# Kernel tuning notes

Measured on AMD Instinct MI355X. Metric: run time of the kernel, lower is better.

Reference implementation:

```python
import jax, jax.numpy as jnp
import numpy as np

N, E, D, R, L = 50000, 250000, 256, 8, 3


def setup_inputs() -> dict:
    key = jax.random.key(0)
    k = jax.random.split(key, 7)
    scale = 1.0 / np.sqrt(D)
    x = jax.random.normal(k[0], (N, D), dtype=jnp.float32)
    edge_index = jax.random.randint(k[1], (2, E), 0, N, dtype=jnp.int64)
    edge_type = jax.random.randint(k[2], (E,), 0, R, dtype=jnp.int64)
    W_rel = jax.random.normal(k[3], (L, R, D, D), dtype=jnp.float32) * scale
    W_root = jax.random.normal(k[4], (L, D, D), dtype=jnp.float32) * scale
    bias = jax.random.normal(k[5], (L, D), dtype=jnp.float32) * 0.02
    return {"x": x, "edge_index": edge_index, "edge_type": edge_type,
            "W_rel": W_rel, "W_root": W_root, "bias": bias}


def reference(x, edge_index, edge_type, W_rel, W_root, bias):
    # RGCNEncoder on the flattened (offset-concatenated) graph:
    # L layers of: h = relu( x @ W_root + b + scatter_add_dst( W_rel[rt] @ x[src] ) )
    src, dst = edge_index[0], edge_index[1]
    n_layers = W_rel.shape[0]
    for l in range(n_layers):  # small fixed layer loop
        # per-relation transform of ALL nodes, then gather per edge by (relation, src)
        xr = jnp.einsum('nd,rde->rne', x, W_rel[l])        # [R, N, D]
        msg = xr[edge_type, src]                           # [E, D] gather
        agg = jax.ops.segment_sum(msg, dst, num_segments=x.shape[0])  # scatter-add
        x = jax.nn.relu(agg + x @ W_root[l] + bias[l])
    return x
```

## Files before the change

kernel.cpp:

```cpp
#include <hip/hip_runtime.h>

#define NN 50000
#define NE 250000
#define DD 256
#define NREL 8
#define NL 3

#define NSRCB ((NN + 127) / 128)
#define NBKT (NREL * NSRCB)

typedef __attribute__((ext_vector_type(8))) short short8;
typedef __attribute__((ext_vector_type(4))) float floatx4;
typedef __attribute__((ext_vector_type(2))) unsigned int u32x2;

#if __has_builtin(__builtin_amdgcn_global_load_lds)
#define GLOAD16(g, l) __builtin_amdgcn_global_load_lds( \
    (__attribute__((address_space(1))) void*)(void*)(g), \
    (__attribute__((address_space(3))) void*)(void*)(l), 16, 0, 0)
#else
#define GLOAD16(g, l) do { *(uint4*)(l) = *(const uint4*)(g); } while (0)
#endif

__device__ inline unsigned short f2bf(float f) {
    unsigned int u = __builtin_bit_cast(unsigned int, f);
    u += 0x7FFFu + ((u >> 16) & 1u);
    return (unsigned short)(u >> 16);
}
__device__ inline float bf2f(unsigned short u) {
    unsigned int x = ((unsigned int)u) << 16;
    return __builtin_bit_cast(float, x);
}

__global__ void zero_ints(int* __restrict__ p, int n) {
    int i = blockIdx.x * blockDim.x + threadIdx.x;
    if (i < n) p[i] = 0;
}

__global__ void hist_bkt(const int* __restrict__ ei, const int* __restrict__ et,
                         int* __restrict__ bktCnt) {
    int e = blockIdx.x * blockDim.x + threadIdx.x;
    if (e < NE) atomicAdd(&bktCnt[et[e] * NSRCB + (ei[e] >> 7)], 1);
}

__global__ __launch_bounds__(256)
void scan_part(const int* __restrict__ cnt, int n, int* __restrict__ blockSums) {
    __shared__ int ps[256];
    const int b = blockIdx.x, t = threadIdx.x;
    const int base = b * 1024 + t * 4;
    int s = 0;
#pragma unroll
    for (int j = 0; j < 4; ++j) s += (base + j < n) ? cnt[base + j] : 0;
    ps[t] = s;
    __syncthreads();
    for (int o = 128; o > 0; o >>= 1) {
        if (t < o) ps[t] += ps[t + o];
        __syncthreads();
    }
    if (t == 0) blockSums[b] = ps[0];
}

__global__ __launch_bounds__(256)
void scan_tops(const int* __restrict__ blockSums, int nb, int* __restrict__ blockOffs) {
    __shared__ int ps[256];
    const int t = threadIdx.x;
    ps[t] = (t < nb) ? blockSums[t] : 0;
    __syncthreads();
    for (int o = 1; o < 256; o <<= 1) {
        int x = (t >= o) ? ps[t - o] : 0;
        __syncthreads();
        ps[t] += x;
        __syncthreads();
    }
    blockOffs[t] = (t == 0) ? 0 : ps[t - 1];
}

__global__ __launch_bounds__(256)
void scan_local(const int* __restrict__ cnt, int n, int total,
                const int* __restrict__ blockOffs,
                int* __restrict__ offs, int* __restrict__ cur) {
    __shared__ int ps[256];
    const int b = blockIdx.x, t = threadIdx.x;
    const int base = b * 1024 + t * 4;
    int v[4];
#pragma unroll
    for (int j = 0; j < 4; ++j) v[j] = (base + j < n) ? cnt[base + j] : 0;
    int s = v[0] + v[1] + v[2] + v[3];
    ps[t] = s;
    __syncthreads();
    for (int o = 1; o < 256; o <<= 1) {
        int x = (t >= o) ? ps[t - o] : 0;
        __syncthreads();
        ps[t] += x;
        __syncthreads();
    }
    int run = blockOffs[b] + ((t == 0) ? 0 : ps[t - 1]);
#pragma unroll
    for (int j = 0; j < 4; ++j) {
        if (base + j < n) { offs[base + j] = run; cur[base + j] = run; run += v[j]; }
    }
    if (b == 0 && t == 0) offs[n] = total;
}

__global__ void mk_reloffs(const int* __restrict__ bktOff, int* __restrict__ relOffs) {
    const int t = threadIdx.x;
    if (t < NREL) relOffs[t] = bktOff[t * NSRCB];
    if (t == 0) relOffs[NREL] = NE;
}

__global__ void scatter_bkt(const int* __restrict__ ei, const int* __restrict__ et,
                            int* __restrict__ bktCur, int* __restrict__ ssrc,
                            int* __restrict__ sdst) {
    int e = blockIdx.x * blockDim.x + threadIdx.x;
    if (e < NE) {
        int s = ei[e];
        int p = atomicAdd(&bktCur[et[e] * NSRCB + (s >> 7)], 1);
        ssrc[p] = s;
        sdst[p] = ei[NE + e];
    }
}

__global__ void hist_dst(const int* __restrict__ sdst, int* __restrict__ dstCnt) {
    int p = blockIdx.x * blockDim.x + threadIdx.x;
    if (p < NE) atomicAdd(&dstCnt[sdst[p]], 1);
}

__global__ void mk_mpos(const int* __restrict__ sdst, int* __restrict__ dstCur,
                        int* __restrict__ mpos) {
    int p = blockIdx.x * blockDim.x + threadIdx.x;
    if (p < NE) mpos[p] = atomicAdd(&dstCur[sdst[p]], 1);
}

__global__ void transpose_bf16(const float* __restrict__ src, unsigned short* __restrict__ dst) {
    __shared__ float t[32][33];
    const size_t mb = (size_t)blockIdx.x * DD * DD;
    const int d0 = blockIdx.y * 32, e0 = blockIdx.z * 32;
    const int tx = threadIdx.x, ty = threadIdx.y;
#pragma unroll
    for (int i = 0; i < 4; ++i)
        t[ty + 8 * i][tx] = src[mb + (size_t)(d0 + ty + 8 * i) * DD + e0 + tx];
    __syncthreads();
#pragma unroll
    for (int i = 0; i < 4; ++i)
        dst[mb + (size_t)(e0 + ty + 8 * i) * DD + d0 + tx] = f2bf(t[tx][ty + 8 * i]);
}

__global__ void conv_bf16(const float4* __restrict__ s, ushort4* __restrict__ d, int n4) {
    int i = blockIdx.x * blockDim.x + threadIdx.x;
    const int stride = gridDim.x * blockDim.x;
    for (; i < n4; i += stride) {
        float4 v = s[i];
        d[i] = make_ushort4(f2bf(v.x), f2bf(v.y), f2bf(v.z), f2bf(v.w));
    }
}

__global__ void relu_convert(float4* __restrict__ p, ushort4* __restrict__ xb, int n4) {
    int i = blockIdx.x * blockDim.x + threadIdx.x;
    const int stride = gridDim.x * blockDim.x;
    for (; i < n4; i += stride) {
        float4 v = p[i];
        v.x = v.x > 0.f ? v.x : 0.f;
        v.y = v.y > 0.f ? v.y : 0.f;
        v.z = v.z > 0.f ? v.z : 0.f;
        v.w = v.w > 0.f ? v.w : 0.f;
        p[i] = v;
        xb[i] = make_ushort4(f2bf(v.x), f2bf(v.y), f2bf(v.z), f2bf(v.w));
    }
}

__global__ __launch_bounds__(256)
void root_gemm_r(const unsigned short* __restrict__ Xb, const unsigned short* __restrict__ WT,
                 const float* __restrict__ bias, float* __restrict__ Cf,
                 unsigned short* __restrict__ Cb, int useB)
{
    __shared__ unsigned short As[128][32];
    __shared__ unsigned short Bs[128][32];
    const int tid = threadIdx.x;
    const int lane = tid & 63;
    const int w = tid >> 6;
    const int wr = w >> 1, wc = w & 1;
    const int m0 = blockIdx.x * 128;
    const int n0 = blockIdx.y * 128;
    const int srow = tid >> 2;
    const int sq = tid & 3;

    floatx4 acc[4][4] = {};

    for (int kt = 0; kt < DD / 32; ++kt) {
        const int k0 = kt * 32;
        int r0 = min(m0 + srow, NN - 1);
        int r1 = min(m0 + srow + 64, NN - 1);
        GLOAD16(&Xb[(size_t)r0 * DD + k0 + sq * 8], &As[srow][sq * 8]);
        GLOAD16(&Xb[(size_t)r1 * DD + k0 + sq * 8], &As[srow + 64][sq * 8]);
        GLOAD16(&WT[(size_t)(n0 + srow) * DD + k0 + sq * 8], &Bs[srow][sq * 8]);
        GLOAD16(&WT[(size_t)(n0 + srow + 64) * DD + k0 + sq * 8], &Bs[srow + 64][sq * 8]);
        __syncthreads();
        short8 a[4], b[4];
#pragma unroll
        for (int mi = 0; mi < 4; ++mi)
            a[mi] = *(const short8*)&As[wr * 64 + mi * 16 + (lane & 15)][(lane >> 4) * 8];
#pragma unroll
        for (int ni = 0; ni < 4; ++ni)
            b[ni] = *(const short8*)&Bs[wc * 64 + ni * 16 + (lane & 15)][(lane >> 4) * 8];
#pragma unroll
        for (int mi = 0; mi < 4; ++mi)
#pragma unroll
            for (int ni = 0; ni < 4; ++ni)
                acc[mi][ni] = __builtin_amdgcn_mfma_f32_16x16x32_bf16(a[mi], b[ni], acc[mi][ni], 0, 0, 0);
        __syncthreads();
    }

    const int cq = lane >> 4;
    const int cn = lane & 15;
#pragma unroll
    for (int mi = 0; mi < 4; ++mi) {
#pragma unroll
        for (int q = 0; q < 4; ++q) {
            int row = m0 + wr * 64 + mi * 16 + cq * 4 + q;
            if (row < NN) {
#pragma unroll
                for (int ni = 0; ni < 4; ++ni) {
                    int col = n0 + wc * 64 + ni * 16 + cn;
                    float val = acc[mi][ni][q] + bias[col];
                    if (useB) Cb[(size_t)row * DD + col] = f2bf(val);
                    else      Cf[(size_t)row * DD + col] = val;
                }
            }
        }
    }
}

__global__ __launch_bounds__(256)
void edge_msgs_m(const unsigned short* __restrict__ Xb, const unsigned short* __restrict__ WTl,
                 const int* __restrict__ ssrc, const int* __restrict__ mpos,
                 const int* __restrict__ relOffs, unsigned short* __restrict__ msgs)
{
    __shared__ unsigned short As[128][32];
    __shared__ unsigned short Bs[128][32];
    __shared__ int srcs[128];
    __shared__ int mposs[128];

    const int t = blockIdx.x;
    int rel = -1, base = 0, cnt = 0, accT = 0;
#pragma unroll
    for (int r = 0; r < NREL; ++r) {
        int s = relOffs[r], e = relOffs[r + 1];
        int nt = (e - s + 127) / 128;
        if (rel < 0 && t < accT + nt) {
            rel = r;
            base = s + (t - accT) * 128;
            cnt = min(128, e - base);
        }
        accT += nt;
    }
    if (rel < 0) return;

    const int tid = threadIdx.x;
    if (tid < 128) {
        int idx = base + tid;
        srcs[tid] = (tid < cnt) ? ssrc[idx] : 0;
        mposs[tid] = (tid < cnt) ? mpos[idx] : 0;
    }
    __syncthreads();

    const unsigned short* WT = WTl + (size_t)rel * DD * DD;

    const int lane = tid & 63;
    const int w = tid >> 6;
    const int wr = w >> 1, wc = w & 1;
    const int n0 = blockIdx.y * 128;
    const int srow = tid >> 2;
    const int sq = tid & 3;

    floatx4 acc[4][4] = {};

    for (int kt = 0; kt < DD / 32; ++kt) {
        const int k0 = kt * 32;
        int r0 = srcs[srow];
        int r1 = srcs[srow + 64];
        GLOAD16(&Xb[(size_t)r0 * DD + k0 + sq * 8], &As[srow][sq * 8]);
        GLOAD16(&Xb[(size_t)r1 * DD + k0 + sq * 8], &As[srow + 64][sq * 8]);
        GLOAD16(&WT[(size_t)(n0 + srow) * DD + k0 + sq * 8], &Bs[srow][sq * 8]);
        GLOAD16(&WT[(size_t)(n0 + srow + 64) * DD + k0 + sq * 8], &Bs[srow + 64][sq * 8]);
        __syncthreads();
        short8 a[4], b[4];
#pragma unroll
        for (int mi = 0; mi < 4; ++mi)
            a[mi] = *(const short8*)&As[wr * 64 + mi * 16 + (lane & 15)][(lane >> 4) * 8];
#pragma unroll
        for (int ni = 0; ni < 4; ++ni)
            b[ni] = *(const short8*)&Bs[wc * 64 + ni * 16 + (lane & 15)][(lane >> 4) * 8];
#pragma unroll
        for (int mi = 0; mi < 4; ++mi)
#pragma unroll
            for (int ni = 0; ni < 4; ++ni)
                acc[mi][ni] = __builtin_amdgcn_mfma_f32_16x16x32_bf16(a[mi], b[ni], acc[mi][ni], 0, 0, 0);
        __syncthreads();
    }

    const int cq = lane >> 4;
    const int cn = lane & 15;
#pragma unroll
    for (int mi = 0; mi < 4; ++mi) {
#pragma unroll
        for (int q = 0; q < 4; ++q) {
            int slot = wr * 64 + mi * 16 + cq * 4 + q;
            if (slot < cnt) {
                size_t mrow = (size_t)mposs[slot] * DD + n0 + wc * 64;
#pragma unroll
                for (int ni = 0; ni < 4; ++ni)
                    msgs[mrow + ni * 16 + cn] = f2bf(acc[mi][ni][q]);
            }
        }
    }
}

__global__ __launch_bounds__(256)
void combine4b(const unsigned short* __restrict__ msgs, const int* __restrict__ dstOffs,
               const unsigned short* __restrict__ rootb, const float* __restrict__ rootf,
               float* __restrict__ out, unsigned short* __restrict__ xb,
               int useRootB, int last)
{
    int v = blockIdx.x * 4 + (threadIdx.x >> 6);
    if (v >= NN) return;
    const int lane = threadIdx.x & 63;
    const size_t rb = (size_t)v * DD + lane * 4;
    float4 a;
    if (useRootB) {
        u32x2 r = *(const u32x2*)&rootb[rb];
        a.x = bf2f((unsigned short)(r.x & 0xffff));
        a.y = bf2f((unsigned short)(r.x >> 16));
        a.z = bf2f((unsigned short)(r.y & 0xffff));
        a.w = bf2f((unsigned short)(r.y >> 16));
    } else {
        a = *(const float4*)&rootf[rb];
    }
    const int b0 = dstOffs[v], b1 = dstOffs[v + 1];
    for (int k = b0; k < b1; ++k) {
        u32x2 m = *(const u32x2*)&msgs[(size_t)k * DD + lane * 4];
        a.x += bf2f((unsigned short)(m.x & 0xffff));
        a.y += bf2f((unsigned short)(m.x >> 16));
        a.z += bf2f((unsigned short)(m.y & 0xffff));
        a.w += bf2f((unsigned short)(m.y >> 16));
    }
    a.x = a.x > 0.f ? a.x : 0.f;
    a.y = a.y > 0.f ? a.y : 0.f;
    a.z = a.z > 0.f ? a.z : 0.f;
    a.w = a.w > 0.f ? a.w : 0.f;
    if (last) {
        *(float4*)&out[rb] = a;
    } else {
        *(ushort4*)&xb[rb] = make_ushort4(f2bf(a.x), f2bf(a.y), f2bf(a.z), f2bf(a.w));
    }
}

__global__ __launch_bounds__(256)
void edge_gemm_mfma(const unsigned short* __restrict__ Xb, const unsigned short* __restrict__ WTl,
                    const int* __restrict__ ssrc, const int* __restrict__ sdst,
                    const int* __restrict__ offsets, float* __restrict__ out)
{
    __shared__ unsigned short As[128][32];
    __shared__ unsigned short Bs[128][32];
    __shared__ int srcs[128];
    __shared__ int dsts[128];

    const int t = blockIdx.x;
    int rel = -1, base = 0, cnt = 0, accT = 0;
#pragma unroll
    for (int r = 0; r < NREL; ++r) {
        int s = offsets[r], e = offsets[r + 1];
        int nt = (e - s + 127) / 128;
        if (rel < 0 && t < accT + nt) {
            rel = r;
            base = s + (t - accT) * 128;
            cnt = min(128, e - base);
        }
        accT += nt;
    }
    if (rel < 0) return;

    const int tid = threadIdx.x;
    if (tid < 128) {
        int idx = base + tid;
        srcs[tid] = (tid < cnt) ? ssrc[idx] : 0;
        dsts[tid] = (tid < cnt) ? sdst[idx] : 0;
    }
    __syncthreads();

    const unsigned short* WT = WTl + (size_t)rel * DD * DD;
    const int lane = tid & 63;
    const int w = tid >> 6;
    const int wr = w >> 1, wc = w & 1;
    const int n0 = blockIdx.y * 128;
    const int srow = tid >> 2;
    const int sq = tid & 3;

    floatx4 acc[4][4] = {};

    for (int kt = 0; kt < DD / 32; ++kt) {
        const int k0 = kt * 32;
        int r0 = srcs[srow];
        int r1 = srcs[srow + 64];
        GLOAD16(&Xb[(size_t)r0 * DD + k0 + sq * 8], &As[srow][sq * 8]);
        GLOAD16(&Xb[(size_t)r1 * DD + k0 + sq * 8], &As[srow + 64][sq * 8]);
        GLOAD16(&WT[(size_t)(n0 + srow) * DD + k0 + sq * 8], &Bs[srow][sq * 8]);
        GLOAD16(&WT[(size_t)(n0 + srow + 64) * DD + k0 + sq * 8], &Bs[srow + 64][sq * 8]);
        __syncthreads();
        short8 a[4], b[4];
#pragma unroll
        for (int mi = 0; mi < 4; ++mi)
            a[mi] = *(const short8*)&As[wr * 64 + mi * 16 + (lane & 15)][(lane >> 4) * 8];
#pragma unroll
        for (int ni = 0; ni < 4; ++ni)
            b[ni] = *(const short8*)&Bs[wc * 64 + ni * 16 + (lane & 15)][(lane >> 4) * 8];
#pragma unroll
        for (int mi = 0; mi < 4; ++mi)
#pragma unroll
            for (int ni = 0; ni < 4; ++ni)
                acc[mi][ni] = __builtin_amdgcn_mfma_f32_16x16x32_bf16(a[mi], b[ni], acc[mi][ni], 0, 0, 0);
        __syncthreads();
    }

    const int cq = lane >> 4;
    const int cn = lane & 15;
#pragma unroll
    for (int mi = 0; mi < 4; ++mi) {
#pragma unroll
        for (int q = 0; q < 4; ++q) {
            int slot = wr * 64 + mi * 16 + cq * 4 + q;
            if (slot < cnt) {
                int d = dsts[slot];
#pragma unroll
                for (int ni = 0; ni < 4; ++ni) {
                    int col = n0 + wc * 64 + ni * 16 + cn;
                    atomicAdd(&out[(size_t)d * DD + col], acc[mi][ni][q]);
                }
            }
        }
    }
}

extern "C" void kernel_launch(void* const* d_in, const int* in_sizes, int n_in,
                              void* d_out, int out_size, void* d_ws, size_t ws_size,
                              hipStream_t stream)
{
    const float* x      = (const float*)d_in[0];
    const int*   ei     = (const int*)d_in[1];
    const int*   et     = (const int*)d_in[2];
    const float* W_rel  = (const float*)d_in[3];
    const float* W_root = (const float*)d_in[4];
    const float* bias   = (const float*)d_in[5];
    float* out = (float*)d_out;

    unsigned char* wsb = (unsigned char*)d_ws;
    size_t off = 0;
    auto alloc = [&](size_t bytes) -> void* {
        void* p = wsb + off;
        off = (off + bytes + 255) & ~(size_t)255;
        return p;
    };
    unsigned short* xb      = (unsigned short*)alloc((size_t)NN * DD * 2);
    unsigned short* wrelT   = (unsigned short*)alloc((size_t)NL * NREL * DD * DD * 2);
    unsigned short* wrootT  = (unsigned short*)alloc((size_t)NL * DD * DD * 2);
    int* ssrc    = (int*)alloc((size_t)NE * 4);
    int* sdst    = (int*)alloc((size_t)NE * 4);
    int* mpos    = (int*)alloc((size_t)NE * 4);
    int* dstOffs = (int*)alloc((size_t)(NN + 1) * 4);
    int* dstCnt  = (int*)alloc((size_t)NN * 4);
    int* dstCur  = (int*)alloc((size_t)NN * 4);
    int* bktCnt  = (int*)alloc((size_t)NBKT * 4);
    int* bktOff  = (int*)alloc((size_t)(NBKT + 1) * 4);
    int* bktCur  = (int*)alloc((size_t)NBKT * 4);
    int* relOffs = (int*)alloc((size_t)(NREL + 1) * 4);
    int* bktSums = (int*)alloc(256 * 4);
    int* bktBOff = (int*)alloc(256 * 4);
    int* dstSums = (int*)alloc(256 * 4);
    int* dstBOff = (int*)alloc(256 * 4);

    const size_t cap = (ws_size > off) ? ws_size - off : 0;
    const size_t needMsgs = (size_t)NE * DD * 2;
    const size_t needRoot = (size_t)NN * DD * 2;
    int mode;
    int useRootB;
    unsigned short* rootb = nullptr;
    unsigned short* msgs = nullptr;
    if (cap >= needMsgs + needRoot + 512) {
        mode = 1; useRootB = 1;
        rootb = (unsigned short*)alloc(needRoot);
        msgs  = (unsigned short*)alloc(needMsgs);
    } else if (cap >= needMsgs) {
        mode = 1; useRootB = 0;
        msgs  = (unsigned short*)alloc(needMsgs);
    } else {
        mode = 0; useRootB = 0;
    }

    const int nbBkt = (NBKT + 1023) / 1024;
    const int nbDst = (NN + 1023) / 1024;

    transpose_bf16<<<dim3(NL * NREL, DD / 32, DD / 32), dim3(32, 8), 0, stream>>>(W_rel, wrelT);
    transpose_bf16<<<dim3(NL, DD / 32, DD / 32), dim3(32, 8), 0, stream>>>(W_root, wrootT);
    conv_bf16<<<2048, 256, 0, stream>>>((const float4*)x, (ushort4*)xb, NN * DD / 4);

    zero_ints<<<(NBKT + 255) / 256, 256, 0, stream>>>(bktCnt, NBKT);
    hist_bkt<<<(NE + 255) / 256, 256, 0, stream>>>(ei, et, bktCnt);
    scan_part<<<nbBkt, 256, 0, stream>>>(bktCnt, NBKT, bktSums);
    scan_tops<<<1, 256, 0, stream>>>(bktSums, nbBkt, bktBOff);
    scan_local<<<nbBkt, 256, 0, stream>>>(bktCnt, NBKT, NE, bktBOff, bktOff, bktCur);
    mk_reloffs<<<1, 64, 0, stream>>>(bktOff, relOffs);
    scatter_bkt<<<(NE + 255) / 256, 256, 0, stream>>>(ei, et, bktCur, ssrc, sdst);

    if (mode == 1) {
        zero_ints<<<(NN + 255) / 256, 256, 0, stream>>>(dstCnt, NN);
        hist_dst<<<(NE + 255) / 256, 256, 0, stream>>>(sdst, dstCnt);
        scan_part<<<nbDst, 256, 0, stream>>>(dstCnt, NN, dstSums);
        scan_tops<<<1, 256, 0, stream>>>(dstSums, nbDst, dstBOff);
        scan_local<<<nbDst, 256, 0, stream>>>(dstCnt, NN, NE, dstBOff, dstOffs, dstCur);
        mk_mpos<<<(NE + 255) / 256, 256, 0, stream>>>(sdst, dstCur, mpos);
    }

    const int ntiles = (NE + 127) / 128 + NREL;
    const int ncomb = (NN + 3) / 4;

    for (int l = 0; l < NL; ++l) {
        const unsigned short* wl = wrelT + (size_t)l * NREL * DD * DD;
        if (mode == 1) {
            root_gemm_r<<<dim3((NN + 127) / 128, DD / 128), 256, 0, stream>>>(
                xb, wrootT + (size_t)l * DD * DD, bias + (size_t)l * DD, out, rootb, useRootB);
            edge_msgs_m<<<dim3(ntiles, 2), 256, 0, stream>>>(xb, wl, ssrc, mpos, relOffs, msgs);
            combine4b<<<ncomb, 256, 0, stream>>>(msgs, dstOffs, rootb, out, out, xb,
                                                 useRootB, (l == NL - 1) ? 1 : 0);
        } else {
            root_gemm_r<<<dim3((NN + 127) / 128, DD / 128), 256, 0, stream>>>(
                xb, wrootT + (size_t)l * DD * DD, bias + (size_t)l * DD, out, nullptr, 0);
            edge_gemm_mfma<<<dim3(ntiles, DD / 128), 256, 0, stream>>>(
                xb, wl, ssrc, sdst, relOffs, out);
            relu_convert<<<2048, 256, 0, stream>>>((float4*)out, (ushort4*)xb, NN * DD / 4);
        }
    }
}
```

Measured before the change: 493.9 us.

## Split edge messages into column halves with ping-pong buffers; swizzle LDS tiles

The edge-message GEMM and the combine step now run once per 128-column half. The message buffer shrinks to NE×128 bf16, which may let it stay in the large last-level cache between write and read. Because the output columns are produced in two passes, the layer input and output are double-buffered (xbA/xbB) so the second half still reads the old activations. An XOR swizzle on the LDS tile layout is also added to both GEMM kernels to reduce bank conflicts on fragment reads. The cost is more kernel launches, the src rows being gathered twice, and the fallback path where the root result is kept in fp32 being removed.

New measurement: 554.1 us. 12.2% more time.

```diff
diff --git a/kernel.cpp b/kernel.cpp
--- a/kernel.cpp
+++ b/kernel.cpp
@@ -182,6 +182,7 @@
     const int n0 = blockIdx.y * 128;
     const int srow = tid >> 2;
     const int sq = tid & 3;
+    const int sq2 = sq ^ ((srow >> 1) & 3);
 
     floatx4 acc[4][4] = {};
 
@@ -189,18 +190,21 @@
         const int k0 = kt * 32;
         int r0 = min(m0 + srow, NN - 1);
         int r1 = min(m0 + srow + 64, NN - 1);
-        GLOAD16(&Xb[(size_t)r0 * DD + k0 + sq * 8], &As[srow][sq * 8]);
-        GLOAD16(&Xb[(size_t)r1 * DD + k0 + sq * 8], &As[srow + 64][sq * 8]);
-        GLOAD16(&WT[(size_t)(n0 + srow) * DD + k0 + sq * 8], &Bs[srow][sq * 8]);
-        GLOAD16(&WT[(size_t)(n0 + srow + 64) * DD + k0 + sq * 8], &Bs[srow + 64][sq * 8]);
-        __syncthreads();
+        GLOAD16(&Xb[(size_t)r0 * DD + k0 + sq2 * 8], &As[srow][sq * 8]);
+        GLOAD16(&Xb[(size_t)r1 * DD + k0 + sq2 * 8], &As[srow + 64][sq * 8]);
+        GLOAD16(&WT[(size_t)(n0 + srow) * DD + k0 + sq2 * 8], &Bs[srow][sq * 8]);
+        GLOAD16(&WT[(size_t)(n0 + srow + 64) * DD + k0 + sq2 * 8], &Bs[srow + 64][sq * 8]);
+        __syncthreads();
+        const int k16 = lane >> 4;
+        const int fr = lane & 15;
+        const int keff = k16 ^ ((fr >> 1) & 3);
         short8 a[4], b[4];
 #pragma unroll
         for (int mi = 0; mi < 4; ++mi)
-            a[mi] = *(const short8*)&As[wr * 64 + mi * 16 + (lane & 15)][(lane >> 4) * 8];
+            a[mi] = *(const short8*)&As[wr * 64 + mi * 16 + fr][keff * 8];
 #pragma unroll
         for (int ni = 0; ni < 4; ++ni)
-            b[ni] = *(const short8*)&Bs[wc * 64 + ni * 16 + (lane & 15)][(lane >> 4) * 8];
+            b[ni] = *(const short8*)&Bs[wc * 64 + ni * 16 + fr][keff * 8];
 #pragma unroll
         for (int mi = 0; mi < 4; ++mi)
 #pragma unroll
@@ -230,9 +234,9 @@
 }
 
 __global__ __launch_bounds__(256)
-void edge_msgs_m(const unsigned short* __restrict__ Xb, const unsigned short* __restrict__ WTl,
+void edge_msgs_h(const unsigned short* __restrict__ Xb, const unsigned short* __restrict__ WTl,
                  const int* __restrict__ ssrc, const int* __restrict__ mpos,
-                 const int* __restrict__ relOffs, unsigned short* __restrict__ msgs)
+                 const int* __restrict__ relOffs, unsigned short* __restrict__ msgs, int h)
 {
     __shared__ unsigned short As[128][32];
     __shared__ unsigned short Bs[128][32];
@@ -267,9 +271,10 @@
     const int lane = tid & 63;
     const int w = tid >> 6;
     const int wr = w >> 1, wc = w & 1;
-    const int n0 = blockIdx.y * 128;
+    const int n0 = h * 128;
     const int srow = tid >> 2;
     const int sq = tid & 3;
+    const int sq2 = sq ^ ((srow >> 1) & 3);
 
     floatx4 acc[4][4] = {};
 
@@ -277,18 +282,21 @@
         const int k0 = kt * 32;
         int r0 = srcs[srow];
         int r1 = srcs[srow + 64];
-        GLOAD16(&Xb[(size_t)r0 * DD + k0 + sq * 8], &As[srow][sq * 8]);
-        GLOAD16(&Xb[(size_t)r1 * DD + k0 + sq * 8], &As[srow + 64][sq * 8]);
-        GLOAD16(&WT[(size_t)(n0 + srow) * DD + k0 + sq * 8], &Bs[srow][sq * 8]);
-        GLOAD16(&WT[(size_t)(n0 + srow + 64) * DD + k0 + sq * 8], &Bs[srow + 64][sq * 8]);
-        __syncthreads();
+        GLOAD16(&Xb[(size_t)r0 * DD + k0 + sq2 * 8], &As[srow][sq * 8]);
+        GLOAD16(&Xb[(size_t)r1 * DD + k0 + sq2 * 8], &As[srow + 64][sq * 8]);
+        GLOAD16(&WT[(size_t)(n0 + srow) * DD + k0 + sq2 * 8], &Bs[srow][sq * 8]);
+        GLOAD16(&WT[(size_t)(n0 + srow + 64) * DD + k0 + sq2 * 8], &Bs[srow + 64][sq * 8]);
+        __syncthreads();
+        const int k16 = lane >> 4;
+        const int fr = lane & 15;
+        const int keff = k16 ^ ((fr >> 1) & 3);
         short8 a[4], b[4];
 #pragma unroll
         for (int mi = 0; mi < 4; ++mi)
-            a[mi] = *(const short8*)&As[wr * 64 + mi * 16 + (lane & 15)][(lane >> 4) * 8];
+            a[mi] = *(const short8*)&As[wr * 64 + mi * 16 + fr][keff * 8];
 #pragma unroll
         for (int ni = 0; ni < 4; ++ni)
-            b[ni] = *(const short8*)&Bs[wc * 64 + ni * 16 + (lane & 15)][(lane >> 4) * 8];
+            b[ni] = *(const short8*)&Bs[wc * 64 + ni * 16 + fr][keff * 8];
 #pragma unroll
         for (int mi = 0; mi < 4; ++mi)
 #pragma unroll
@@ -305,7 +313,7 @@
         for (int q = 0; q < 4; ++q) {
             int slot = wr * 64 + mi * 16 + cq * 4 + q;
             if (slot < cnt) {
-                size_t mrow = (size_t)mposs[slot] * DD + n0 + wc * 64;
+                size_t mrow = (size_t)mposs[slot] * 128 + wc * 64;
 #pragma unroll
                 for (int ni = 0; ni < 4; ++ni)
                     msgs[mrow + ni * 16 + cn] = f2bf(acc[mi][ni][q]);
@@ -315,41 +323,30 @@
 }
 
 __global__ __launch_bounds__(256)
-void combine4b(const unsigned short* __restrict__ msgs, const int* __restrict__ dstOffs,
-               const unsigned short* __restrict__ rootb, const float* __restrict__ rootf,
-               float* __restrict__ out, unsigned short* __restrict__ xb,
-               int useRootB, int last)
+void combine_h(const unsigned short* __restrict__ msgs, const int* __restrict__ dstOffs,
+               const unsigned short* __restrict__ rootb, float* __restrict__ out,
+               unsigned short* __restrict__ xbOut, int h, int last)
 {
     int v = blockIdx.x * 4 + (threadIdx.x >> 6);
     if (v >= NN) return;
     const int lane = threadIdx.x & 63;
-    const size_t rb = (size_t)v * DD + lane * 4;
-    float4 a;
-    if (useRootB) {
-        u32x2 r = *(const u32x2*)&rootb[rb];
-        a.x = bf2f((unsigned short)(r.x & 0xffff));
-        a.y = bf2f((unsigned short)(r.x >> 16));
-        a.z = bf2f((unsigned short)(r.y & 0xffff));
-        a.w = bf2f((unsigned short)(r.y >> 16));
-    } else {
-        a = *(const float4*)&rootf[rb];
-    }
+    const size_t rb = (size_t)v * DD + h * 128 + lane * 2;
+    unsigned int r = *(const unsigned int*)&rootb[rb];
+    float a0 = bf2f((unsigned short)(r & 0xffff));
+    float a1 = bf2f((unsigned short)(r >> 16));
     const int b0 = dstOffs[v], b1 = dstOffs[v + 1];
     for (int k = b0; k < b1; ++k) {
-        u32x2 m = *(const u32x2*)&msgs[(size_t)k * DD + lane * 4];
-        a.x += bf2f((unsigned short)(m.x & 0xffff));
-        a.y += bf2f((unsigned short)(m.x >> 16));
-        a.z += bf2f((unsigned short)(m.y & 0xffff));
-        a.w += bf2f((unsigned short)(m.y >> 16));
-    }
-    a.x = a.x > 0.f ? a.x : 0.f;
-    a.y = a.y > 0.f ? a.y : 0.f;
-    a.z = a.z > 0.f ? a.z : 0.f;
-    a.w = a.w > 0.f ? a.w : 0.f;
+        unsigned int m = *(const unsigned int*)&msgs[(size_t)k * 128 + lane * 2];
+        a0 += bf2f((unsigned short)(m & 0xffff));
+        a1 += bf2f((unsigned short)(m >> 16));
+    }
+    a0 = a0 > 0.f ? a0 : 0.f;
+    a1 = a1 > 0.f ? a1 : 0.f;
     if (last) {
-        *(float4*)&out[rb] = a;
+        *(float2*)&out[rb] = make_float2(a0, a1);
     } else {
-        *(ushort4*)&xb[rb] = make_ushort4(f2bf(a.x), f2bf(a.y), f2bf(a.z), f2bf(a.w));
+        unsigned int p = (unsigned int)f2bf(a0) | ((unsigned int)f2bf(a1) << 16);
+        *(unsigned int*)&xbOut[rb] = p;
     }
 }
 
@@ -458,7 +455,7 @@
         off = (off + bytes + 255) & ~(size_t)255;
         return p;
     };
-    unsigned short* xb      = (unsigned short*)alloc((size_t)NN * DD * 2);
+    unsigned short* xbA     = (unsigned short*)alloc((size_t)NN * DD * 2);
     unsigned short* wrelT   = (unsigned short*)alloc((size_t)NL * NREL * DD * DD * 2);
     unsigned short* wrootT  = (unsigned short*)alloc((size_t)NL * DD * DD * 2);
     int* ssrc    = (int*)alloc((size_t)NE * 4);
@@ -477,21 +474,20 @@
     int* dstBOff = (int*)alloc(256 * 4);
 
     const size_t cap = (ws_size > off) ? ws_size - off : 0;
-    const size_t needMsgs = (size_t)NE * DD * 2;
+    const size_t needMsgs = (size_t)NE * 128 * 2;
     const size_t needRoot = (size_t)NN * DD * 2;
+    const size_t needXbB  = (size_t)NN * DD * 2;
     int mode;
-    int useRootB;
+    unsigned short* xbB = nullptr;
     unsigned short* rootb = nullptr;
     unsigned short* msgs = nullptr;
-    if (cap >= needMsgs + needRoot + 512) {
-        mode = 1; useRootB = 1;
+    if (cap >= needMsgs + needRoot + needXbB + 1024) {
+        mode = 1;
+        xbB   = (unsigned short*)alloc(needXbB);
         rootb = (unsigned short*)alloc(needRoot);
         msgs  = (unsigned short*)alloc(needMsgs);
-    } else if (cap >= needMsgs) {
-        mode = 1; useRootB = 0;
-        msgs  = (unsigned short*)alloc(needMsgs);
     } else {
-        mode = 0; useRootB = 0;
+        mode = 0;
     }
 
     const int nbBkt = (NBKT + 1023) / 1024;
@@ -499,7 +495,7 @@
 
     transpose_bf16<<<dim3(NL * NREL, DD / 32, DD / 32), dim3(32, 8), 0, stream>>>(W_rel, wrelT);
     transpose_bf16<<<dim3(NL, DD / 32, DD / 32), dim3(32, 8), 0, stream>>>(W_root, wrootT);
-    conv_bf16<<<2048, 256, 0, stream>>>((const float4*)x, (ushort4*)xb, NN * DD / 4);
+    conv_bf16<<<2048, 256, 0, stream>>>((const float4*)x, (ushort4*)xbA, NN * DD / 4);
 
     zero_ints<<<(NBKT + 255) / 256, 256, 0, stream>>>(bktCnt, NBKT);
     hist_bkt<<<(NE + 255) / 256, 256, 0, stream>>>(ei, et, bktCnt);
@@ -524,17 +520,23 @@
     for (int l = 0; l < NL; ++l) {
         const unsigned short* wl = wrelT + (size_t)l * NREL * DD * DD;
         if (mode == 1) {
+            unsigned short* xbIn  = (l & 1) ? xbB : xbA;
+            unsigned short* xbOut = (l & 1) ? xbA : xbB;
+            const int last = (l == NL - 1) ? 1 : 0;
             root_gemm_r<<<dim3((NN + 127) / 128, DD / 128), 256, 0, stream>>>(
-                xb, wrootT + (size_t)l * DD * DD, bias + (size_t)l * DD, out, rootb, useRootB);
-            edge_msgs_m<<<dim3(ntiles, 2), 256, 0, stream>>>(xb, wl, ssrc, mpos, relOffs, msgs);
-            combine4b<<<ncomb, 256, 0, stream>>>(msgs, dstOffs, rootb, out, out, xb,
-                                                 useRootB, (l == NL - 1) ? 1 : 0);
+                xbIn, wrootT + (size_t)l * DD * DD, bias + (size_t)l * DD, out, rootb, 1);
+            for (int h = 0; h < 2; ++h) {
+                edge_msgs_h<<<dim3(ntiles), 256, 0, stream>>>(
+                    xbIn, wl, ssrc, mpos, relOffs, msgs, h);
+                combine_h<<<ncomb, 256, 0, stream>>>(
+                    msgs, dstOffs, rootb, out, xbOut, h, last);
+            }
         } else {
             root_gemm_r<<<dim3((NN + 127) / 128, DD / 128), 256, 0, stream>>>(
-                xb, wrootT + (size_t)l * DD * DD, bias + (size_t)l * DD, out, nullptr, 0);
+                xbA, wrootT + (size_t)l * DD * DD, bias + (size_t)l * DD, out, nullptr, 0);
             edge_gemm_mfma<<<dim3(ntiles, DD / 128), 256, 0, stream>>>(
-                xb, wl, ssrc, sdst, relOffs, out);
-            relu_convert<<<2048, 256, 0, stream>>>((float4*)out, (ushort4*)xb, NN * DD / 4);
+                xbA, wl, ssrc, sdst, relOffs, out);
+            relu_convert<<<2048, 256, 0, stream>>>((float4*)out, (ushort4*)xbA, NN * DD / 4);
         }
     }
 }
```
